# Performance work log

Measured on AMD Instinct MI355X. Metric: run time of the kernel, lower is better.

Reference implementation:

```python
import jax, jax.numpy as jnp
import numpy as np

B, H, S, D = 1, 16, 2048, 64
G, HK = 8, 2              # num_head_groups, head_kernel_size
QK, KK = 6, 11            # query_kernel_size, key_kernel_size
EPS = 1e-5


def setup_inputs() -> dict:
    key = jax.random.key(0)
    ks = jax.random.split(key, 6)
    q = jax.random.normal(ks[0], (B, H, S, D), jnp.float32)
    k = jax.random.normal(ks[1], (B, H, S, D), jnp.float32)
    v = jax.random.normal(ks[2], (B, H, S, D), jnp.float32)
    # depthwise conv weight [C_out=H, C_in/groups=1, QK, KK]: identity at center + noise
    conv_w = 0.02 * jax.random.normal(ks[3], (H, 1, QK, KK), jnp.float32)
    conv_w = conv_w.at[:, 0, QK // 2, KK // 2].add(1.0)
    conv_b = 0.01 * jax.random.normal(ks[4], (H,), jnp.float32)
    # head mixing weights [G, HK, HK]: identity init + noise
    head_mix = jnp.broadcast_to(jnp.eye(HK, dtype=jnp.float32), (G, HK, HK)) \
        + 0.1 * jax.random.normal(ks[5], (G, HK, HK), jnp.float32)
    ln_gamma = jnp.ones((D,), jnp.float32)
    ln_beta = jnp.zeros((D,), jnp.float32)
    return {"q": q, "k": k, "v": v, "conv_w": conv_w, "conv_b": conv_b,
            "head_mix": head_mix, "ln_gamma": ln_gamma, "ln_beta": ln_beta}


def _mta_forward(q, k, v, conv_w, conv_b, head_mix, ln_gamma, ln_beta):
    b, h, s, d = q.shape
    scale = 1.0 / np.sqrt(d).astype(np.float32)
    scores = jnp.einsum('bhsd,bhkd->bhsk', q, k) * scale          # [B,H,S,S]
    mask = jnp.triu(jnp.ones((s, s), dtype=bool), 1)              # strict upper = future
    # key-query convolution with double masking (paper eq. 4)
    masked = jnp.where(mask, 0.0, scores)
    # torch padding='same' for even kernel 6: left=2, right=3; for 11: (5,5)
    conv = jax.lax.conv_general_dilated(
        masked, conv_w, window_strides=(1, 1),
        padding=[(2, 3), (5, 5)],
        dimension_numbers=('NCHW', 'OIHW', 'NCHW'),
        feature_group_count=h)
    conv = conv + conv_b[None, :, None, None]
    final = jnp.where(mask, -1e9, conv)
    w = jax.nn.softmax(final, axis=-1)
    # post-softmax head mixing within groups of HK heads
    wg = w.reshape(b, G, HK, s, s)
    mixed = jnp.einsum('bgisk,gij->bgjsk', wg, head_mix).reshape(b, h, s, s)
    out = jnp.einsum('bhsk,bhkd->bhsd', mixed, v)                 # [B,H,S,D]
    # LayerNorm over head_dim (torch uses biased variance)
    mu = jnp.mean(out, axis=-1, keepdims=True)
    var = jnp.mean(jnp.square(out - mu), axis=-1, keepdims=True)
    return (out - mu) * jax.lax.rsqrt(var + EPS) * ln_gamma + ln_beta


def reference(q, k, v, conv_w, conv_b, head_mix, ln_gamma, ln_beta):
    return _mta_forward(q, k, v, conv_w, conv_b, head_mix, ln_gamma, ln_beta)
```

## Files before the change

### kernel.cpp

```cpp
#include <hip/hip_runtime.h>
#include <math.h>

#define SS 2048
#define QP 72
#define KP 72
#define VP 72
#define SFP 88
#define PP 72

typedef __attribute__((ext_vector_type(8))) _Float16 h8v;
typedef __attribute__((ext_vector_type(2))) __fp16 p2v;
typedef __attribute__((ext_vector_type(4))) float f4v;

__device__ __forceinline__ unsigned long long pack4h(float4 v) {
    union { p2v h[2]; unsigned long long u; } t;
    t.h[0] = __builtin_amdgcn_cvt_pkrtz(v.x, v.y);
    t.h[1] = __builtin_amdgcn_cvt_pkrtz(v.z, v.w);
    return t.u;
}

__global__ __launch_bounds__(512, 2)
void mta_v11(const float* __restrict__ Q, const float* __restrict__ K,
             const float* __restrict__ V, const float* __restrict__ CW,
             const float* __restrict__ CB, const float* __restrict__ MIX,
             const float* __restrict__ GAM, const float* __restrict__ BET,
             float* __restrict__ OUT)
{
    __shared__ __align__(16) _Float16 sQ[96 * QP];
    __shared__ __align__(16) _Float16 sK[2][160 * KP];
    __shared__ __align__(16) _Float16 sVt[2][128 * VP];
    __shared__ __align__(16) _Float16 sSf[96 * SFP];
    __shared__ __align__(16) _Float16 sP[64 * PP];
    __shared__ float sResc[2][32];
    __shared__ float sL[2][32];
    __shared__ float sW2[2][66];
    __shared__ float sB2[2];

    const int tid = threadIdx.x;
    const int g = blockIdx.x & 7;
    const int u = blockIdx.x >> 3;

    const int wv = tid >> 6, lane = tid & 63;
    const int lrow = lane & 15;
    const int lk8 = (lane >> 4) << 3;
    const int crow4 = (lane >> 4) << 2;

    const int i_pv = wv >> 2, j_pv = (wv >> 1) & 1, kh = wv & 1;
    const int hC = wv >> 1, mtw = wv & 1;

    for (int idx = tid; idx < 132; idx += 512) {
        int h = idx >= 66;
        sW2[h][idx - (h ? 66 : 0)] = CW[(2 * g + h) * 66 + (idx - (h ? 66 : 0))];
    }
    if (tid < 2) sB2[tid] = CB[2 * g + tid];
    const float mixc = MIX[g * 4 + i_pv * 2 + j_pv];
    __syncthreads();

    h8v tf[6];
    float biasC = 0.f;
    if (wv < 4) {
        biasC = sB2[hC];
#pragma unroll
        for (int i = 0; i < 6; ++i)
#pragma unroll
            for (int e = 0; e < 8; ++e) {
                int d = lk8 + e - lrow;
                tf[i][e] = (d >= 0 && d <= 10) ? (_Float16)sW2[hC][i * 11 + d] : (_Float16)0.f;
            }
    }

    const float4* Q4 = (const float4*)Q;
    const float4* K4 = (const float4*)K;
    const float4* V4 = (const float4*)V;

    for (int ti = 0; ti < 2; ++ti) {
        const int tile = ti ? u : (63 - u);
        const int q0 = tile << 5;
        __syncthreads();

        for (int idx = tid; idx < 1536; idx += 512) {
            int h = idx >= 768;
            int rem = idx - (h ? 768 : 0);
            int e = rem >> 4, d4 = rem & 15;
            int r = q0 - 2 + e;
            float4 val = make_float4(0.f, 0.f, 0.f, 0.f);
            if (r >= 0 && r < SS) val = Q4[((2 * g + h) * SS + r) * 16 + d4];
            *(unsigned long long*)&sQ[(h * 48 + e) * QP + (d4 << 2)] = pack4h(val);
        }
        for (int idx = tid; idx < 2560; idx += 512) {
            int h = idx >= 1280;
            int rem = idx - (h ? 1280 : 0);
            int e = rem >> 4, d4 = rem & 15;
            int c = -5 + e;
            float4 val = make_float4(0.f, 0.f, 0.f, 0.f);
            if (e < 74 && c >= 0 && c < SS) val = K4[((2 * g + h) * SS + c) * 16 + d4];
            *(unsigned long long*)&sK[0][(h * 80 + e) * KP + (d4 << 2)] = pack4h(val);
        }
        for (int idx = tid; idx < 2048; idx += 512) {
            int h = idx >> 10, d4 = (idx >> 6) & 15, kk = idx & 63;
            float4 val = V4[((2 * g + h) * SS + kk) * 16 + d4];
            int d = d4 << 2;
            sVt[0][(h * 64 + d + 0) * VP + kk] = (_Float16)val.x;
            sVt[0][(h * 64 + d + 1) * VP + kk] = (_Float16)val.y;
            sVt[0][(h * 64 + d + 2) * VP + kk] = (_Float16)val.z;
            sVt[0][(h * 64 + d + 3) * VP + kk] = (_Float16)val.w;
        }

        f4v acc[2][4];
#pragma unroll
        for (int mt = 0; mt < 2; ++mt)
#pragma unroll
            for (int nt = 0; nt < 4; ++nt) acc[mt][nt] = f4v{0.f, 0.f, 0.f, 0.f};
        float m_run = -INFINITY, l_run = 0.f;
        int cur = 0;

        __syncthreads();

        const int iters = (tile >> 1) + 1;
        for (int it = 0; it < iters; ++it) {
            const int k0 = it << 6;
            const bool pf = (it + 1) < iters;
            const int k0n = (it + 1) << 6;
            const int nxt = cur ^ 1;

#pragma unroll
            for (int jj = 0; jj < 4; ++jj) {
                int job = wv + (jj << 3);
                if (job < 30) {
                    int h = job >= 15;
                    int r15 = job - (h ? 15 : 0);
                    int mt = (r15 >= 10) ? 2 : ((r15 >= 5) ? 1 : 0);
                    int nt = r15 - 5 * mt;
                    const _Float16* ap = &sQ[(h * 48 + mt * 16 + lrow) * QP + lk8];
                    const _Float16* bp = &sK[cur][(h * 80 + nt * 16 + lrow) * KP + lk8];
                    f4v c = f4v{0.f, 0.f, 0.f, 0.f};
                    c = __builtin_amdgcn_mfma_f32_16x16x32_f16(*(const h8v*)ap,
                                                               *(const h8v*)bp, c, 0, 0, 0);
                    c = __builtin_amdgcn_mfma_f32_16x16x32_f16(*(const h8v*)(ap + 32),
                                                               *(const h8v*)(bp + 32), c, 0, 0, 0);
                    int col = nt * 16 + lrow;
                    int cab = k0 - 5 + col;
                    int rbase = mt * 16 + crow4;
#pragma unroll
                    for (int r = 0; r < 4; ++r)
                        sSf[(h * 48 + rbase + r) * SFP + col] =
                            (_Float16)((cab <= q0 - 2 + rbase + r) ? c[r] * 0.125f : 0.f);
                }
            }
            __syncthreads();

            if (wv < 4) {
                f4v cc[4];
                __builtin_amdgcn_s_setprio(1);
#pragma unroll
                for (int ct = 0; ct < 4; ++ct) {
                    f4v c = f4v{biasC, biasC, biasC, biasC};
#pragma unroll
                    for (int i = 0; i < 6; ++i) {
                        h8v b = *(const h8v*)&sSf[(hC * 48 + mtw * 16 + i + lrow) * SFP + ct * 16 + lk8];
                        c = __builtin_amdgcn_mfma_f32_16x16x32_f16(tf[i], b, c, 0, 0, 0);
                    }
                    cc[ct] = c;
                }
                __builtin_amdgcn_s_setprio(0);
                const int qrow = q0 + mtw * 16 + lrow;
                float tm = -INFINITY;
#pragma unroll
                for (int ct = 0; ct < 4; ++ct)
#pragma unroll
                    for (int r = 0; r < 4; ++r) {
                        int ca = k0 + ct * 16 + crow4 + r;
                        float v = cc[ct][r];
                        if (ca > qrow) v = -1e9f;
                        cc[ct][r] = v;
                        tm = fmaxf(tm, v);
                    }
                tm = fmaxf(tm, __shfl_xor(tm, 16));
                tm = fmaxf(tm, __shfl_xor(tm, 32));
                float mnew = fmaxf(m_run, tm);
                float resc = __expf(m_run - mnew);
                m_run = mnew;
                float ps = 0.f;
#pragma unroll
                for (int ct = 0; ct < 4; ++ct)
#pragma unroll
                    for (int r = 0; r < 4; ++r) {
                        float p = __expf(cc[ct][r] - mnew);
                        cc[ct][r] = p;
                        ps += p;
                    }
                ps += __shfl_xor(ps, 16);
                ps += __shfl_xor(ps, 32);
                l_run = l_run * resc + ps;
                if ((lane >> 4) == 0) sResc[hC][mtw * 16 + lrow] = resc;
#pragma unroll
                for (int ct = 0; ct < 4; ++ct) {
                    union { p2v h[2]; unsigned long long u; } t;
                    t.h[0] = __builtin_amdgcn_cvt_pkrtz(cc[ct][0], cc[ct][1]);
                    t.h[1] = __builtin_amdgcn_cvt_pkrtz(cc[ct][2], cc[ct][3]);
                    *(unsigned long long*)&sP[(hC * 32 + mtw * 16 + lrow) * PP + ct * 16 + crow4] = t.u;
                }
            } else if (pf) {
                const int stid = ((wv - 4) << 6) + lane;
                float4 kreg[10], vreg[8];
#pragma unroll
                for (int n = 0; n < 10; ++n) {
                    int idx = stid + (n << 8);
                    int h = idx >= 1280;
                    int rem = idx - (h ? 1280 : 0);
                    int e = rem >> 4, d4 = rem & 15;
                    int c = k0n - 5 + e;
                    kreg[n] = make_float4(0.f, 0.f, 0.f, 0.f);
                    if (e < 74 && c >= 0 && c < SS)
                        kreg[n] = K4[((2 * g + h) * SS + c) * 16 + d4];
                }
#pragma unroll
                for (int n = 0; n < 8; ++n) {
                    int idx = stid + (n << 8);
                    int h = idx >> 10, d4 = (idx >> 6) & 15, kk = idx & 63;
                    vreg[n] = V4[((2 * g + h) * SS + k0n + kk) * 16 + d4];
                }
#pragma unroll
                for (int n = 0; n < 10; ++n) {
                    int idx = stid + (n << 8);
                    int h = idx >= 1280;
                    int rem = idx - (h ? 1280 : 0);
                    int e = rem >> 4, d4 = rem & 15;
                    *(unsigned long long*)&sK[nxt][(h * 80 + e) * KP + (d4 << 2)] = pack4h(kreg[n]);
                }
#pragma unroll
                for (int n = 0; n < 8; ++n) {
                    int idx = stid + (n << 8);
                    int h = idx >> 10, d4 = (idx >> 6) & 15, kk = idx & 63;
                    int d = d4 << 2;
                    sVt[nxt][(h * 64 + d + 0) * VP + kk] = (_Float16)vreg[n].x;
                    sVt[nxt][(h * 64 + d + 1) * VP + kk] = (_Float16)vreg[n].y;
                    sVt[nxt][(h * 64 + d + 2) * VP + kk] = (_Float16)vreg[n].z;
                    sVt[nxt][(h * 64 + d + 3) * VP + kk] = (_Float16)vreg[n].w;
                }
            }
            __syncthreads();

            {
#pragma unroll
                for (int mt = 0; mt < 2; ++mt)
#pragma unroll
                    for (int r = 0; r < 4; ++r) {
                        float f = sResc[i_pv][mt * 16 + crow4 + r];
#pragma unroll
                        for (int nt = 0; nt < 4; ++nt) acc[mt][nt][r] *= f;
                    }
#pragma unroll
                for (int mt = 0; mt < 2; ++mt) {
                    h8v a = *(const h8v*)&sP[(i_pv * 32 + mt * 16 + lrow) * PP + (kh << 5) + lk8];
#pragma unroll
                    for (int nt = 0; nt < 4; ++nt) {
                        h8v b = *(const h8v*)&sVt[cur][(j_pv * 64 + nt * 16 + lrow) * VP + (kh << 5) + lk8];
                        acc[mt][nt] = __builtin_amdgcn_mfma_f32_16x16x32_f16(a, b, acc[mt][nt], 0, 0, 0);
                    }
                }
            }
            cur = nxt;
        }

        if (wv < 4 && (lane >> 4) == 0) sL[hC][mtw * 16 + lrow] = l_run;
        __syncthreads();

        float* sO = (float*)&sK[0][0];
#pragma unroll
        for (int st = 0; st < 4; ++st) {
            if (i_pv == (st >> 1) && kh == (st & 1)) {
#pragma unroll
                for (int mt = 0; mt < 2; ++mt)
#pragma unroll
                    for (int r = 0; r < 4; ++r) {
                        int row = mt * 16 + crow4 + r;
                        float cc2 = mixc / sL[i_pv][row];
#pragma unroll
                        for (int nt = 0; nt < 4; ++nt) {
                            int col = nt * 16 + lrow;
                            float val = acc[mt][nt][r] * cc2;
                            if (st == 0) sO[(j_pv * 32 + row) * 68 + col] = val;
                            else         sO[(j_pv * 32 + row) * 68 + col] += val;
                        }
                    }
            }
            __syncthreads();
        }

        {
            const float4* G4 = (const float4*)GAM;
            const float4* B4 = (const float4*)BET;
#pragma unroll
            for (int itl = 0; itl < 2; ++itl) {
                int pidx = tid + (itl << 9);
                int d4 = pidx & 15, rowj = pidx >> 4;
                int j = rowj >> 5, qq = rowj & 31;
                float4 o = *(const float4*)&sO[rowj * 68 + (d4 << 2)];
                float s1 = o.x + o.y + o.z + o.w;
                float s2 = o.x * o.x + o.y * o.y + o.z * o.z + o.w * o.w;
#pragma unroll
                for (int off = 1; off < 16; off <<= 1) {
                    s1 += __shfl_xor(s1, off);
                    s2 += __shfl_xor(s2, off);
                }
                float mean = s1 * (1.f / 64.f);
                float var = s2 * (1.f / 64.f) - mean * mean;
                float rs = rsqrtf(var + 1e-5f);
                float4 gm = G4[d4], bt = B4[d4];
                float4 ov;
                ov.x = (o.x - mean) * rs * gm.x + bt.x;
                ov.y = (o.y - mean) * rs * gm.y + bt.y;
                ov.z = (o.z - mean) * rs * gm.z + bt.z;
                ov.w = (o.w - mean) * rs * gm.w + bt.w;
                *(float4*)&OUT[(((2 * g + j) * SS + q0 + qq) << 6) + (d4 << 2)] = ov;
            }
        }
    }
}

extern "C" void kernel_launch(void* const* d_in, const int* in_sizes, int n_in,
                              void* d_out, int out_size, void* d_ws, size_t ws_size,
                              hipStream_t stream) {
    const float* q = (const float*)d_in[0];
    const float* k = (const float*)d_in[1];
    const float* v = (const float*)d_in[2];
    const float* cw = (const float*)d_in[3];
    const float* cb = (const float*)d_in[4];
    const float* mix = (const float*)d_in[5];
    const float* gam = (const float*)d_in[6];
    const float* bet = (const float*)d_in[7];
    float* out = (float*)d_out;

    dim3 grid(8 * 32);
    dim3 block(512);
    hipLaunchKernelGGL(mta_v11, grid, block, 0, stream,
                       q, k, v, cw, cb, mix, gam, bet, out);
}
```

Measured before the change: 105.3 us.

## Warp-specialize QK/conv/softmax and PV waves with a one-iteration software pipeline

Waves 0-3 now compute their own QK tiles, the conv and the softmax, redundantly recomputing one overlapping row tile so no block barrier is needed between QK and conv. Waves 4-7 prefetch K/V and run the PV MFMA for the previous iteration, with P and the rescale factors double-buffered and V triple-buffered. This removes one __syncthreads per iteration and overlaps softmax with PV. In exchange, PV work is concentrated on half the waves, some QK MFMAs are duplicated, and LDS use grows.

```diff
diff --git a/kernel.cpp b/kernel.cpp
--- a/kernel.cpp
+++ b/kernel.cpp
@@ -20,7 +20,7 @@
 }
 
 __global__ __launch_bounds__(512, 2)
-void mta_v11(const float* __restrict__ Q, const float* __restrict__ K,
+void mta_v13(const float* __restrict__ Q, const float* __restrict__ K,
              const float* __restrict__ V, const float* __restrict__ CW,
              const float* __restrict__ CB, const float* __restrict__ MIX,
              const float* __restrict__ GAM, const float* __restrict__ BET,
@@ -28,10 +28,10 @@
 {
     __shared__ __align__(16) _Float16 sQ[96 * QP];
     __shared__ __align__(16) _Float16 sK[2][160 * KP];
-    __shared__ __align__(16) _Float16 sVt[2][128 * VP];
+    __shared__ __align__(16) _Float16 sVt[3][128 * VP];
     __shared__ __align__(16) _Float16 sSf[96 * SFP];
-    __shared__ __align__(16) _Float16 sP[64 * PP];
-    __shared__ float sResc[2][32];
+    __shared__ __align__(16) _Float16 sP[2][64 * PP];
+    __shared__ float sResc[2][2][32];
     __shared__ float sL[2][32];
     __shared__ float sW2[2][66];
     __shared__ float sB2[2];
@@ -45,8 +45,9 @@
     const int lk8 = (lane >> 4) << 3;
     const int crow4 = (lane >> 4) << 2;
 
-    const int i_pv = wv >> 2, j_pv = (wv >> 1) & 1, kh = wv & 1;
-    const int hC = wv >> 1, mtw = wv & 1;
+    const int sw = (wv >= 4) ? (wv - 4) : 0;
+    const int i_pv = sw >> 1, j_pv = sw & 1;
+    const int hC = (wv >> 1) & 1, mtw = wv & 1;
 
     for (int idx = tid; idx < 132; idx += 512) {
         int h = idx >= 66;
@@ -112,44 +113,38 @@
 #pragma unroll
             for (int nt = 0; nt < 4; ++nt) acc[mt][nt] = f4v{0.f, 0.f, 0.f, 0.f};
         float m_run = -INFINITY, l_run = 0.f;
-        int cur = 0;
 
         __syncthreads();
 
         const int iters = (tile >> 1) + 1;
         for (int it = 0; it < iters; ++it) {
             const int k0 = it << 6;
+            const int cur2 = it & 1;
             const bool pf = (it + 1) < iters;
             const int k0n = (it + 1) << 6;
-            const int nxt = cur ^ 1;
-
-#pragma unroll
-            for (int jj = 0; jj < 4; ++jj) {
-                int job = wv + (jj << 3);
-                if (job < 30) {
-                    int h = job >= 15;
-                    int r15 = job - (h ? 15 : 0);
-                    int mt = (r15 >= 10) ? 2 : ((r15 >= 5) ? 1 : 0);
-                    int nt = r15 - 5 * mt;
-                    const _Float16* ap = &sQ[(h * 48 + mt * 16 + lrow) * QP + lk8];
-                    const _Float16* bp = &sK[cur][(h * 80 + nt * 16 + lrow) * KP + lk8];
-                    f4v c = f4v{0.f, 0.f, 0.f, 0.f};
-                    c = __builtin_amdgcn_mfma_f32_16x16x32_f16(*(const h8v*)ap,
-                                                               *(const h8v*)bp, c, 0, 0, 0);
-                    c = __builtin_amdgcn_mfma_f32_16x16x32_f16(*(const h8v*)(ap + 32),
-                                                               *(const h8v*)(bp + 32), c, 0, 0, 0);
-                    int col = nt * 16 + lrow;
-                    int cab = k0 - 5 + col;
+
+            if (wv < 4) {
+#pragma unroll
+                for (int mtt = 0; mtt < 2; ++mtt) {
+                    int mt = mtw + mtt;
+                    const _Float16* ap = &sQ[(hC * 48 + mt * 16 + lrow) * QP + lk8];
+                    h8v a0 = *(const h8v*)ap;
+                    h8v a1 = *(const h8v*)(ap + 32);
                     int rbase = mt * 16 + crow4;
 #pragma unroll
-                    for (int r = 0; r < 4; ++r)
-                        sSf[(h * 48 + rbase + r) * SFP + col] =
-                            (_Float16)((cab <= q0 - 2 + rbase + r) ? c[r] * 0.125f : 0.f);
-                }
-            }
-            __syncthreads();
-
-            if (wv < 4) {
+                    for (int nt = 0; nt < 5; ++nt) {
+                        const _Float16* bp = &sK[cur2][(hC * 80 + nt * 16 + lrow) * KP + lk8];
+                        f4v c = f4v{0.f, 0.f, 0.f, 0.f};
+                        c = __builtin_amdgcn_mfma_f32_16x16x32_f16(a0, *(const h8v*)bp, c, 0, 0, 0);
+                        c = __builtin_amdgcn_mfma_f32_16x16x32_f16(a1, *(const h8v*)(bp + 32), c, 0, 0, 0);
+                        int col = nt * 16 + lrow;
+                        int cab = k0 - 5 + col;
+#pragma unroll
+                        for (int r = 0; r < 4; ++r)
+                            sSf[(hC * 48 + rbase + r) * SFP + col] =
+                                (_Float16)((cab <= q0 - 2 + rbase + r) ? c[r] * 0.125f : 0.f);
+                    }
+                }
                 f4v cc[4];
                 __builtin_amdgcn_s_setprio(1);
 #pragma unroll
@@ -192,84 +187,116 @@
                 ps += __shfl_xor(ps, 16);
                 ps += __shfl_xor(ps, 32);
                 l_run = l_run * resc + ps;
-                if ((lane >> 4) == 0) sResc[hC][mtw * 16 + lrow] = resc;
+                if ((lane >> 4) == 0) sResc[cur2][hC][mtw * 16 + lrow] = resc;
 #pragma unroll
                 for (int ct = 0; ct < 4; ++ct) {
                     union { p2v h[2]; unsigned long long u; } t;
                     t.h[0] = __builtin_amdgcn_cvt_pkrtz(cc[ct][0], cc[ct][1]);
                     t.h[1] = __builtin_amdgcn_cvt_pkrtz(cc[ct][2], cc[ct][3]);
-                    *(unsigned long long*)&sP[(hC * 32 + mtw * 16 + lrow) * PP + ct * 16 + crow4] = t.u;
-                }
-            } else if (pf) {
+                    *(unsigned long long*)&sP[cur2][(hC * 32 + mtw * 16 + lrow) * PP + ct * 16 + crow4] = t.u;
+                }
+            } else {
                 const int stid = ((wv - 4) << 6) + lane;
                 float4 kreg[10], vreg[8];
-#pragma unroll
-                for (int n = 0; n < 10; ++n) {
-                    int idx = stid + (n << 8);
-                    int h = idx >= 1280;
-                    int rem = idx - (h ? 1280 : 0);
-                    int e = rem >> 4, d4 = rem & 15;
-                    int c = k0n - 5 + e;
-                    kreg[n] = make_float4(0.f, 0.f, 0.f, 0.f);
-                    if (e < 74 && c >= 0 && c < SS)
-                        kreg[n] = K4[((2 * g + h) * SS + c) * 16 + d4];
-                }
-#pragma unroll
-                for (int n = 0; n < 8; ++n) {
-                    int idx = stid + (n << 8);
-                    int h = idx >> 10, d4 = (idx >> 6) & 15, kk = idx & 63;
-                    vreg[n] = V4[((2 * g + h) * SS + k0n + kk) * 16 + d4];
-                }
-#pragma unroll
-                for (int n = 0; n < 10; ++n) {
-                    int idx = stid + (n << 8);
-                    int h = idx >= 1280;
-                    int rem = idx - (h ? 1280 : 0);
-                    int e = rem >> 4, d4 = rem & 15;
-                    *(unsigned long long*)&sK[nxt][(h * 80 + e) * KP + (d4 << 2)] = pack4h(kreg[n]);
-                }
-#pragma unroll
-                for (int n = 0; n < 8; ++n) {
-                    int idx = stid + (n << 8);
-                    int h = idx >> 10, d4 = (idx >> 6) & 15, kk = idx & 63;
-                    int d = d4 << 2;
-                    sVt[nxt][(h * 64 + d + 0) * VP + kk] = (_Float16)vreg[n].x;
-                    sVt[nxt][(h * 64 + d + 1) * VP + kk] = (_Float16)vreg[n].y;
-                    sVt[nxt][(h * 64 + d + 2) * VP + kk] = (_Float16)vreg[n].z;
-                    sVt[nxt][(h * 64 + d + 3) * VP + kk] = (_Float16)vreg[n].w;
+                if (pf) {
+#pragma unroll
+                    for (int n = 0; n < 10; ++n) {
+                        int idx = stid + (n << 8);
+                        int h = idx >= 1280;
+                        int rem = idx - (h ? 1280 : 0);
+                        int e = rem >> 4, d4 = rem & 15;
+                        int c = k0n - 5 + e;
+                        kreg[n] = make_float4(0.f, 0.f, 0.f, 0.f);
+                        if (e < 74 && c >= 0 && c < SS)
+                            kreg[n] = K4[((2 * g + h) * SS + c) * 16 + d4];
+                    }
+#pragma unroll
+                    for (int n = 0; n < 8; ++n) {
+                        int idx = stid + (n << 8);
+                        int h = idx >> 10, d4 = (idx >> 6) & 15, kk = idx & 63;
+                        vreg[n] = V4[((2 * g + h) * SS + k0n + kk) * 16 + d4];
+                    }
+                }
+                if (it > 0) {
+                    const int pcur = (it - 1) & 1;
+                    const int pv = (it - 1) % 3;
+#pragma unroll
+                    for (int mt = 0; mt < 2; ++mt)
+#pragma unroll
+                        for (int r = 0; r < 4; ++r) {
+                            float f = sResc[pcur][i_pv][mt * 16 + crow4 + r];
+#pragma unroll
+                            for (int nt = 0; nt < 4; ++nt) acc[mt][nt][r] *= f;
+                        }
+#pragma unroll
+                    for (int kh = 0; kh < 2; ++kh)
+#pragma unroll
+                        for (int mt = 0; mt < 2; ++mt) {
+                            h8v a = *(const h8v*)&sP[pcur][(i_pv * 32 + mt * 16 + lrow) * PP + (kh << 5) + lk8];
+#pragma unroll
+                            for (int nt = 0; nt < 4; ++nt) {
+                                h8v b = *(const h8v*)&sVt[pv][(j_pv * 64 + nt * 16 + lrow) * VP + (kh << 5) + lk8];
+                                acc[mt][nt] = __builtin_amdgcn_mfma_f32_16x16x32_f16(a, b, acc[mt][nt], 0, 0, 0);
+                            }
+                        }
+                }
+                if (pf) {
+                    const int kb = (it + 1) & 1;
+                    const int vb = (it + 1) % 3;
+#pragma unroll
+                    for (int n = 0; n < 10; ++n) {
+                        int idx = stid + (n << 8);
+                        int h = idx >= 1280;
+                        int rem = idx - (h ? 1280 : 0);
+                        int e = rem >> 4, d4 = rem & 15;
+                        *(unsigned long long*)&sK[kb][(h * 80 + e) * KP + (d4 << 2)] = pack4h(kreg[n]);
+                    }
+#pragma unroll
+                    for (int n = 0; n < 8; ++n) {
+                        int idx = stid + (n << 8);
+                        int h = idx >> 10, d4 = (idx >> 6) & 15, kk = idx & 63;
+                        int d = d4 << 2;
+                        sVt[vb][(h * 64 + d + 0) * VP + kk] = (_Float16)vreg[n].x;
+                        sVt[vb][(h * 64 + d + 1) * VP + kk] = (_Float16)vreg[n].y;
+                        sVt[vb][(h * 64 + d + 2) * VP + kk] = (_Float16)vreg[n].z;
+                        sVt[vb][(h * 64 + d + 3) * VP + kk] = (_Float16)vreg[n].w;
+                    }
                 }
             }
             __syncthreads();
-
-            {
-#pragma unroll
-                for (int mt = 0; mt < 2; ++mt)
-#pragma unroll
-                    for (int r = 0; r < 4; ++r) {
-                        float f = sResc[i_pv][mt * 16 + crow4 + r];
-#pragma unroll
-                        for (int nt = 0; nt < 4; ++nt) acc[mt][nt][r] *= f;
-                    }
+        }
+
+        if (wv < 4) {
+            if ((lane >> 4) == 0) sL[hC][mtw * 16 + lrow] = l_run;
+        } else {
+            const int pcur = (iters - 1) & 1;
+            const int pv = (iters - 1) % 3;
+#pragma unroll
+            for (int mt = 0; mt < 2; ++mt)
+#pragma unroll
+                for (int r = 0; r < 4; ++r) {
+                    float f = sResc[pcur][i_pv][mt * 16 + crow4 + r];
+#pragma unroll
+                    for (int nt = 0; nt < 4; ++nt) acc[mt][nt][r] *= f;
+                }
+#pragma unroll
+            for (int kh = 0; kh < 2; ++kh)
 #pragma unroll
                 for (int mt = 0; mt < 2; ++mt) {
-                    h8v a = *(const h8v*)&sP[(i_pv * 32 + mt * 16 + lrow) * PP + (kh << 5) + lk8];
+                    h8v a = *(const h8v*)&sP[pcur][(i_pv * 32 + mt * 16 + lrow) * PP + (kh << 5) + lk8];
 #pragma unroll
                     for (int nt = 0; nt < 4; ++nt) {
-                        h8v b = *(const h8v*)&sVt[cur][(j_pv * 64 + nt * 16 + lrow) * VP + (kh << 5) + lk8];
+                        h8v b = *(const h8v*)&sVt[pv][(j_pv * 64 + nt * 16 + lrow) * VP + (kh << 5) + lk8];
                         acc[mt][nt] = __builtin_amdgcn_mfma_f32_16x16x32_f16(a, b, acc[mt][nt], 0, 0, 0);
                     }
                 }
-            }
-            cur = nxt;
-        }
-
-        if (wv < 4 && (lane >> 4) == 0) sL[hC][mtw * 16 + lrow] = l_run;
+        }
         __syncthreads();
 
         float* sO = (float*)&sK[0][0];
 #pragma unroll
-        for (int st = 0; st < 4; ++st) {
-            if (i_pv == (st >> 1) && kh == (st & 1)) {
+        for (int st = 0; st < 2; ++st) {
+            if (wv >= 4 && i_pv == st) {
 #pragma unroll
                 for (int mt = 0; mt < 2; ++mt)
 #pragma unroll
@@ -334,6 +361,6 @@
 
     dim3 grid(8 * 32);
     dim3 block(512);
-    hipLaunchKernelGGL(mta_v11, grid, block, 0, stream,
+    hipLaunchKernelGGL(mta_v13, grid, block, 0, stream,
                        q, k, v, cw, cb, mix, gam, bet, out);
 }
```

New measurement: 133.1 us. 26.3% more time.
